# Optimization experiments

Measured on AMD Instinct MI355X. Metric: run time of the kernel, lower is better.

Reference implementation:

```python
import jax, jax.numpy as jnp
import numpy as np

# static multi-scale config (Deformable-DETR encoder, 1024x1024 image, strides 8/16/32/64)
SPATIAL_SHAPES = np.array([[128, 128], [64, 64], [32, 32], [16, 16]])  # (L, 2) = (h, w)
NUM_HEADS, NUM_LEVELS, NUM_POINTS = 8, 4, 4
EMBED, HEAD_DIM = 256, 32
NUM_KEYS = int(SPATIAL_SHAPES.prod(-1).sum())  # 21760


def _grid_sample(img, grid):
    """Bilinear grid_sample, padding_mode='zeros', align_corners=False.
    img: (BH, C, H, W); grid: (BH, Nq, P, 2) in [-1,1] -> (BH, C, Nq, P)."""
    BH, C, H, W = img.shape
    gx = (grid[..., 0] + 1.0) * (W / 2) - 0.5
    gy = (grid[..., 1] + 1.0) * (H / 2) - 0.5
    x0f, y0f = jnp.floor(gx), jnp.floor(gy)
    wx, wy = gx - x0f, gy - y0f
    x0, y0 = x0f.astype(jnp.int32), y0f.astype(jnp.int32)
    flat = img.reshape(BH, C, H * W)

    def gather(xi, yi, w):
        valid = (xi >= 0) & (xi < W) & (yi >= 0) & (yi < H)
        idx = jnp.clip(yi, 0, H - 1) * W + jnp.clip(xi, 0, W - 1)
        g = jnp.take_along_axis(flat, idx.reshape(BH, 1, -1), axis=2)
        g = g.reshape(BH, C, xi.shape[1], xi.shape[2])
        return g * (w * valid)[:, None]

    return (gather(x0, y0, (1 - wx) * (1 - wy)) + gather(x0 + 1, y0, wx * (1 - wy))
            + gather(x0, y0 + 1, (1 - wx) * wy) + gather(x0 + 1, y0 + 1, wx * wy))


def setup_inputs() -> dict:
    key = jax.random.key(0)
    ks = jax.random.split(key, 12)
    bs, nq = 1, NUM_KEYS
    s = 1.0 / np.sqrt(EMBED)
    return {
        "query": jax.random.normal(ks[0], (bs, nq, EMBED), jnp.float32),
        "query_pos": jax.random.normal(ks[1], (bs, nq, EMBED), jnp.float32),
        "value": jax.random.normal(ks[2], (bs, NUM_KEYS, EMBED), jnp.float32),
        "reference_points": jax.random.uniform(ks[3], (bs, nq, NUM_LEVELS, 2), jnp.float32),
        "spatial_shapes": jnp.asarray(SPATIAL_SHAPES, jnp.int32),
        "W_value": jax.random.normal(ks[4], (EMBED, EMBED), jnp.float32) * s,
        "b_value": jnp.zeros((EMBED,), jnp.float32),
        "W_off": jax.random.normal(ks[5], (NUM_HEADS * NUM_LEVELS * NUM_POINTS * 2, EMBED), jnp.float32) * 0.01,
        "b_off": jax.random.normal(ks[6], (NUM_HEADS * NUM_LEVELS * NUM_POINTS * 2,), jnp.float32),
        "W_attn": jax.random.normal(ks[7], (NUM_HEADS * NUM_LEVELS * NUM_POINTS, EMBED), jnp.float32) * s,
        "b_attn": jnp.zeros((NUM_HEADS * NUM_LEVELS * NUM_POINTS,), jnp.float32),
        "W_out": jax.random.normal(ks[8], (EMBED, EMBED), jnp.float32) * s,
        "b_out": jnp.zeros((EMBED,), jnp.float32),
    }


def reference(query, query_pos, value, reference_points, spatial_shapes,
              W_value, b_value, W_off, b_off, W_attn, b_attn, W_out, b_out):
    bs, nq, _ = query.shape
    identity = query
    q = query + query_pos  # pos_add
    v = value @ W_value.T + b_value  # value_proj: (bs, nk, E)
    v = v.reshape(bs, -1, NUM_HEADS, HEAD_DIM)

    offsets = (q @ W_off.T + b_off).reshape(bs, nq, NUM_HEADS, NUM_LEVELS, NUM_POINTS, 2)
    attn = (q @ W_attn.T + b_attn).reshape(bs, nq, NUM_HEADS, NUM_LEVELS * NUM_POINTS)
    attn = jax.nn.softmax(attn, axis=-1).reshape(bs, nq, NUM_HEADS, NUM_LEVELS, NUM_POINTS)

    # offset_normalizer = (w, h) per level; ref points are 2D -> loc = ref + off/norm
    normalizer = jnp.asarray(SPATIAL_SHAPES[:, ::-1].copy(), query.dtype)  # (L, 2)
    loc = reference_points[:, :, None, :, None, :] + offsets / normalizer[None, None, None, :, None, :]
    grids = 2.0 * loc - 1.0  # (bs, nq, H, L, P, 2)

    starts = np.concatenate([[0], np.cumsum(SPATIAL_SHAPES.prod(-1))])
    sampled = []
    for lvl in range(NUM_LEVELS):
        H_, W_ = int(SPATIAL_SHAPES[lvl, 0]), int(SPATIAL_SHAPES[lvl, 1])
        v_l = v[:, int(starts[lvl]):int(starts[lvl + 1])]  # (bs, H*W, heads, Dh)
        v_l = v_l.transpose(0, 2, 3, 1).reshape(bs * NUM_HEADS, HEAD_DIM, H_, W_)
        g_l = grids[:, :, :, lvl].transpose(0, 2, 1, 3, 4).reshape(bs * NUM_HEADS, nq, NUM_POINTS, 2)
        sampled.append(_grid_sample(v_l, g_l))  # (bs*H, Dh, nq, P)
    sampled = jnp.concatenate(sampled, axis=-1)  # (bs*H, Dh, nq, L*P)

    aw = attn.transpose(0, 2, 1, 3, 4).reshape(bs * NUM_HEADS, 1, nq, NUM_LEVELS * NUM_POINTS)
    out = (sampled * aw).sum(-1).reshape(bs, NUM_HEADS * HEAD_DIM, nq).transpose(0, 2, 1)
    out = out @ W_out.T + b_out  # output_proj
    return out + identity  # residual (dropout is identity at eval)
```

## Files before the change

### kernel.cpp

```cpp
#include <hip/hip_runtime.h>
#include <hip/hip_bf16.h>
#include <math.h>
#include <type_traits>

#define K_DIM 256
using bf16 = __hip_bfloat16;

typedef __attribute__((ext_vector_type(8))) short s8v;
typedef __attribute__((ext_vector_type(4))) float f4v;

__device__ __forceinline__ float b2f(unsigned short u) {
    return __uint_as_float(((unsigned)u) << 16);
}
__device__ __forceinline__ unsigned short f2b(float f) {
    unsigned u = __float_as_uint(f);
    unsigned r = 0x7FFFu + ((u >> 16) & 1u);
    return (unsigned short)((u + r) >> 16);
}
__device__ __forceinline__ float  ld1(const float* p) { return *p; }
__device__ __forceinline__ float  ld1(const bf16*  p) { return b2f(*(const unsigned short*)p); }
__device__ __forceinline__ void   st1(float* p, float v) { *p = v; }
__device__ __forceinline__ void   st1(bf16*  p, float v) { *(unsigned short*)p = f2b(v); }
__device__ __forceinline__ float4 ld4(const float* p) { return *(const float4*)p; }
__device__ __forceinline__ float4 ld4(const bf16*  p) {
    ushort4 u = *(const ushort4*)p;
    return make_float4(b2f(u.x), b2f(u.y), b2f(u.z), b2f(u.w));
}
__device__ __forceinline__ s8v ldw8(const bf16* p) { return *(const s8v*)p; }

__device__ __forceinline__ bool detect_bf16(const unsigned* __restrict__ qw) {
    unsigned w = qw[threadIdx.x & 63];
    unsigned t = (w >> 8) & 0x7F;
    bool hit = (t >= 0x3Bu) && (t <= 0x42u);
    unsigned long long m = __ballot(hit);
    return __popcll(m) >= 32;
}

#define P1_TOTAL 164480
__global__ __launch_bounds__(256) void k_prep1(
    const unsigned* __restrict__ qd,
    const void* wv, const void* wo, const void* wa,
    const void* bv, const void* bo, const void* ba, bf16* __restrict__ dst)
{
    const bool isb = detect_bf16(qd);
    const int i4 = (blockIdx.x * 256 + threadIdx.x) * 4;
    if (i4 >= P1_TOTAL) return;
    const void* src; int off;
    if      (i4 < 65536)  { src = wv; off = i4; }
    else if (i4 < 131072) { src = wo; off = i4 - 65536; }
    else if (i4 < 163840) { src = wa; off = i4 - 131072; }
    else if (i4 < 164096) { src = bv; off = i4 - 163840; }
    else if (i4 < 164352) { src = bo; off = i4 - 164096; }
    else                  { src = ba; off = i4 - 164352; }
    if (isb) {
        *(ushort4*)(dst + i4) = *(const ushort4*)((const unsigned short*)src + off);
    } else {
        float4 v = *(const float4*)((const float*)src + off);
        *(ushort4*)(dst + i4) = make_ushort4(f2b(v.x), f2b(v.y), f2b(v.z), f2b(v.w));
    }
}

#define P2_TOTAL 65792
__global__ __launch_bounds__(256) void k_prep2(
    const unsigned* __restrict__ qd,
    const void* wout, const void* bout, bf16* __restrict__ dst)
{
    const bool isb = detect_bf16(qd);
    const int i4 = (blockIdx.x * 256 + threadIdx.x) * 4;
    if (i4 >= P2_TOTAL) return;
    const void* src; int off;
    if (i4 < 65536) { src = wout; off = i4; }
    else            { src = bout; off = i4 - 65536; }
    if (isb) {
        *(ushort4*)(dst + i4) = *(const ushort4*)((const unsigned short*)src + off);
    } else {
        float4 v = *(const float4*)((const float*)src + off);
        *(ushort4*)(dst + i4) = make_ushort4(f2b(v.x), f2b(v.y), f2b(v.z), f2b(v.w));
    }
}

template<typename AT, typename RT, typename CT, int NFRAG, bool ADD_A2, bool SPLIT,
         bool ADD_RES, bool HMAJOR, bool HM2, bool A1HM>
__device__ __forceinline__ void mfma_gemm_body(
    unsigned short* __restrict__ As,
    const AT* __restrict__ A1, const AT* __restrict__ A2,
    const bf16* __restrict__ W1, const bf16* __restrict__ bias1, CT* __restrict__ C1, int N1,
    const bf16* __restrict__ W2, const bf16* __restrict__ bias2, bf16* __restrict__ C2, int N2,
    const RT* __restrict__ Res, int Mtot)
{
    const int tid = threadIdx.x;
    const int bm = blockIdx.x * 32;

    {
        const AT* t1 = A1 + (size_t)bm * K_DIM;
        if constexpr (!ADD_A2 && std::is_same<AT, bf16>::value) {
            #pragma unroll
            for (int j = 0; j < 4; ++j) {
                const int e = j * 2048 + tid * 8;
                const int row = e >> 8, col = e & 255;
                const bf16* src;
                if constexpr (A1HM)
                    src = (const bf16*)A1 +
                          ((size_t)(col >> 5) * (size_t)Mtot + (size_t)(bm + row)) * 32 + (col & 31);
                else
                    src = t1 + e;
                *(s8v*)&As[row * 264 + col] = *(const s8v*)src;
            }
        } else {
            const AT* t2 = ADD_A2 ? (A2 + (size_t)bm * K_DIM) : (const AT*)0;
            #pragma unroll
            for (int j = 0; j < 8; ++j) {
                const int e = j * 1024 + tid * 4;
                float4 v = ld4(t1 + e);
                if (ADD_A2) {
                    float4 w2 = ld4(t2 + e);
                    v.x += w2.x; v.y += w2.y; v.z += w2.z; v.w += w2.w;
                }
                const int row = e >> 8, col = e & 255;
                *(ushort4*)&As[row * 264 + col] =
                    make_ushort4(f2b(v.x), f2b(v.y), f2b(v.z), f2b(v.w));
            }
        }
    }
    __syncthreads();

    const int wv = tid >> 6;
    const int lane = tid & 63;
    const int n15 = lane & 15;
    const int quad = lane >> 4;

    const bf16* Wr[NFRAG];
    int col[NFRAG];
    #pragma unroll
    for (int f = 0; f < NFRAG; ++f) {
        const int c = (wv * NFRAG + f) * 16 + n15;
        col[f] = c;
        if (SPLIT && c >= N1) Wr[f] = W2 + (size_t)(c - N1) * K_DIM;
        else                  Wr[f] = W1 + (size_t)c * K_DIM;
    }

    const f4v zz = {0.f, 0.f, 0.f, 0.f};
    f4v acc[2][NFRAG];
    #pragma unroll
    for (int mi = 0; mi < 2; ++mi)
        #pragma unroll
        for (int f = 0; f < NFRAG; ++f) acc[mi][f] = zz;

    #pragma unroll
    for (int kk = 0; kk < 8; ++kk) {
        const int k0 = kk * 32 + quad * 8;
        s8v b[NFRAG];
        #pragma unroll
        for (int f = 0; f < NFRAG; ++f) b[f] = ldw8(Wr[f] + k0);
        s8v a[2];
        #pragma unroll
        for (int mi = 0; mi < 2; ++mi)
            a[mi] = *(const s8v*)&As[(mi * 16 + n15) * 264 + k0];
        #pragma unroll
        for (int mi = 0; mi < 2; ++mi)
            #pragma unroll
            for (int f = 0; f < NFRAG; ++f)
                acc[mi][f] = __builtin_amdgcn_mfma_f32_16x16x32_bf16(a[mi], b[f], acc[mi][f], 0, 0, 0);
    }

    #pragma unroll
    for (int f = 0; f < NFRAG; ++f) {
        const int c = col[f];
        const bool hi = SPLIT && (c >= N1);
        const int cc = hi ? (c - N1) : c;
        const float bv = hi ? ld1(bias2 + cc) : ld1(bias1 + c);
        size_t hbase = 0;
        if (HMAJOR) hbase = (size_t)(c >> 5) * (size_t)Mtot * 32 + (c & 31);
        size_t hbase2 = 0;
        if (HM2) hbase2 = (size_t)(cc >> 4) * (size_t)Mtot * 16 + (cc & 15);
        #pragma unroll
        for (int mi = 0; mi < 2; ++mi)
            #pragma unroll
            for (int r = 0; r < 4; ++r) {
                const int m = bm + mi * 16 + quad * 4 + r;
                float v = acc[mi][f][r] + bv;
                if (ADD_RES) v += ld1(Res + (size_t)m * N1 + c);
                if (hi) {
                    if (HM2) st1(C2 + hbase2 + (size_t)m * 16, v);
                    else     st1(C2 + (size_t)m * N2 + cc, v);
                }
                else if (HMAJOR) st1(C1 + hbase + (size_t)m * 32, v);
                else             st1(C1 + (size_t)m * N1 + c, v);
            }
    }
}

template<int NFRAG, bool ADD_A2, bool SPLIT, bool HMAJOR, bool HM2>
__global__ __launch_bounds__(256) void k_gemm(
    const unsigned* __restrict__ qd, const void* A1, const void* A2,
    const bf16* W1, const bf16* b1, bf16* C1, int N1,
    const bf16* W2, const bf16* b2, bf16* C2, int N2, int Mtot)
{
    __shared__ unsigned short As[32 * 264];
    if (detect_bf16(qd))
        mfma_gemm_body<bf16, float, bf16, NFRAG, ADD_A2, SPLIT, false, HMAJOR, HM2, false>(As,
            (const bf16*)A1, (const bf16*)A2, W1, b1, C1, N1, W2, b2, C2, N2, nullptr, Mtot);
    else
        mfma_gemm_body<float, float, bf16, NFRAG, ADD_A2, SPLIT, false, HMAJOR, HM2, false>(As,
            (const float*)A1, (const float*)A2, W1, b1, C1, N1, W2, b2, C2, N2, nullptr, Mtot);
}

__global__ __launch_bounds__(256) void k_gemm_final(
    const unsigned* __restrict__ qd, const bf16* A1,
    const bf16* W, const bf16* bias, const void* Res, void* C, int Mtot)
{
    __shared__ unsigned short As[32 * 264];
    if (detect_bf16(qd))
        mfma_gemm_body<bf16, bf16, bf16, 4, false, false, true, false, false, true>(As,
            A1, nullptr, W, bias, (bf16*)C, 256,
            nullptr, nullptr, nullptr, 0, (const bf16*)Res, Mtot);
    else
        mfma_gemm_body<bf16, float, float, 4, false, false, true, false, false, true>(As,
            A1, nullptr, W, bias, (float*)C, 256,
            nullptr, nullptr, nullptr, 0, (const float*)Res, Mtot);
}

struct SampLds {
    float    swgt[16][32][4];
    unsigned sidx[16][32][4];
};

__global__ __launch_bounds__(256) void k_sample(
    const unsigned* __restrict__ qd, const bf16* __restrict__ vproj,
    bf16* __restrict__ osb, const bf16* __restrict__ logits,
    const void* __restrict__ refp, int Mtot)
{
    __shared__ SampLds L;
    const bool isb = detect_bf16(qd);
    const int t  = threadIdx.x;
    const int p  = t >> 3;
    const int dg = t & 7;
    const int head = blockIdx.x & 7;
    const int qc   = blockIdx.x >> 3;
    const int q = qc * 32 + p;
    const size_t hm = (size_t)head * (size_t)Mtot;

    float f0, f1, f2, f3;
    {
        ushort4 u = *(const ushort4*)(osb + (hm + q) * 32 + dg * 4);
        f0 = b2f(u.x); f1 = b2f(u.y); f2 = b2f(u.z); f3 = b2f(u.w);
    }

    float p0, p1;
    {
        ushort2 lu = *(const ushort2*)(logits + (hm + q) * 16 + dg * 2);
        float l0 = b2f(lu.x), l1 = b2f(lu.y);
        float mx = fmaxf(l0, l1);
        mx = fmaxf(mx, __shfl_xor(mx, 1));
        mx = fmaxf(mx, __shfl_xor(mx, 2));
        mx = fmaxf(mx, __shfl_xor(mx, 4));
        float e0 = __expf(l0 - mx), e1 = __expf(l1 - mx);
        float s = e0 + e1;
        s += __shfl_xor(s, 1);
        s += __shfl_xor(s, 2);
        s += __shfl_xor(s, 4);
        const float inv = 1.f / s;
        p0 = e0 * inv; p1 = e1 * inv;
    }

    const int lv = dg >> 1;
    float rx, ry;
    if (isb) {
        rx = ld1((const bf16*)refp + (size_t)q * 8 + 2 * lv);
        ry = ld1((const bf16*)refp + (size_t)q * 8 + 2 * lv + 1);
    } else {
        rx = ld1((const float*)refp + (size_t)q * 8 + 2 * lv);
        ry = ld1((const float*)refp + (size_t)q * 8 + 2 * lv + 1);
    }

    #pragma unroll
    for (int tt = 0; tt < 2; ++tt) {
        const int i = dg * 2 + tt;
        const int l = i >> 2;
        const int WW = 128 >> l;
        const int st = (l == 0) ? 0 : (l == 1) ? 16384 : (l == 2) ? 20480 : 21504;
        const float ox = tt ? f2 : f0;
        const float oy = tt ? f3 : f1;
        const float aw = tt ? p1 : p0;
        const float gx = rx * (float)WW + ox - 0.5f;
        const float gy = ry * (float)WW + oy - 0.5f;
        const float x0f = floorf(gx);
        const float y0f = floorf(gy);
        const float wx = gx - x0f;
        const float wy = gy - y0f;
        const int x0 = (int)x0f;
        const int y0 = (int)y0f;
        const float vx0 = (x0 >= 0 && x0 < WW) ? 1.f : 0.f;
        const float vx1 = (x0 + 1 >= 0 && x0 + 1 < WW) ? 1.f : 0.f;
        const float vy0 = (y0 >= 0 && y0 < WW) ? 1.f : 0.f;
        const float vy1 = (y0 + 1 >= 0 && y0 + 1 < WW) ? 1.f : 0.f;
        const int xc0 = min(max(x0, 0), WW - 1);
        const int xc1 = min(max(x0 + 1, 0), WW - 1);
        const int yc0 = min(max(y0, 0), WW - 1);
        const int yc1 = min(max(y0 + 1, 0), WW - 1);
        *(float4*)L.swgt[i][p] = make_float4(
            (1.f - wx) * (1.f - wy) * aw * vx0 * vy0,
            wx * (1.f - wy) * aw * vx1 * vy0,
            (1.f - wx) * wy * aw * vx0 * vy1,
            wx * wy * aw * vx1 * vy1);
        *(uint4*)L.sidx[i][p] = make_uint4(
            (unsigned)(st + yc0 * WW + xc0) * 64u,
            (unsigned)(st + yc0 * WW + xc1) * 64u,
            (unsigned)(st + yc1 * WW + xc0) * 64u,
            (unsigned)(st + yc1 * WW + xc1) * 64u);
    }
    __syncthreads();

    const unsigned hb = (unsigned)(hm * 64) + (unsigned)dg * 8u;
    const char* vb = (const char*)vproj;
    float a0 = 0.f, a1 = 0.f, a2 = 0.f, a3 = 0.f;
    #pragma unroll
    for (int i = 0; i < 16; ++i) {
        const uint4  iv = *(const uint4*)L.sidx[i][p];
        const float4 wv = *(const float4*)L.swgt[i][p];
        {
            ushort4 pv = *(const ushort4*)(vb + (size_t)(iv.x + hb));
            a0 = fmaf(wv.x, b2f(pv.x), a0); a1 = fmaf(wv.x, b2f(pv.y), a1);
            a2 = fmaf(wv.x, b2f(pv.z), a2); a3 = fmaf(wv.x, b2f(pv.w), a3);
        }
        {
            ushort4 pv = *(const ushort4*)(vb + (size_t)(iv.y + hb));
            a0 = fmaf(wv.y, b2f(pv.x), a0); a1 = fmaf(wv.y, b2f(pv.y), a1);
            a2 = fmaf(wv.y, b2f(pv.z), a2); a3 = fmaf(wv.y, b2f(pv.w), a3);
        }
        {
            ushort4 pv = *(const ushort4*)(vb + (size_t)(iv.z + hb));
            a0 = fmaf(wv.z, b2f(pv.x), a0); a1 = fmaf(wv.z, b2f(pv.y), a1);
            a2 = fmaf(wv.z, b2f(pv.z), a2); a3 = fmaf(wv.z, b2f(pv.w), a3);
        }
        {
            ushort4 pv = *(const ushort4*)(vb + (size_t)(iv.w + hb));
            a0 = fmaf(wv.w, b2f(pv.x), a0); a1 = fmaf(wv.w, b2f(pv.y), a1);
            a2 = fmaf(wv.w, b2f(pv.z), a2); a3 = fmaf(wv.w, b2f(pv.w), a3);
        }
    }
    *(ushort4*)(osb + (hm + q) * 32 + dg * 4) =
        make_ushort4(f2b(a0), f2b(a1), f2b(a2), f2b(a3));
}

extern "C" void kernel_launch(void* const* d_in, const int* in_sizes, int n_in,
                              void* d_out, int out_size, void* d_ws, size_t ws_size,
                              hipStream_t stream) {
    const void* query     = d_in[0];
    const void* query_pos = d_in[1];
    const void* value     = d_in[2];
    const void* refp      = d_in[3];
    const void* W_value = d_in[5];
    const void* b_value = d_in[6];
    const void* W_off   = d_in[7];
    const void* b_off   = d_in[8];
    const void* W_attn  = d_in[9];
    const void* b_attn  = d_in[10];
    const void* W_out   = d_in[11];
    const void* b_out   = d_in[12];
    const unsigned* qd = (const unsigned*)d_in[0];

    const int M = in_sizes[0] / 256;
    char* wsb = (char*)d_ws;

    bf16* vproj = (bf16*)wsb;
    bf16* osb   = (bf16*)(wsb + (size_t)M * 512);
    bf16* logit = (bf16*)d_out;
    bf16* wc1   = (bf16*)((char*)d_out + (8u << 20));
    const bf16* c_wv = wc1;
    const bf16* c_wo = wc1 + 65536;
    const bf16* c_wa = wc1 + 131072;
    const bf16* c_bv = wc1 + 163840;
    const bf16* c_bo = wc1 + 164096;
    const bf16* c_ba = wc1 + 164352;
    bf16* wc2 = vproj;

    dim3 blk(256, 1, 1);
    dim3 g32((unsigned)(M / 32), 1, 1);
    dim3 gs((unsigned)(M / 4), 1, 1);

    k_prep1<<<dim3((P1_TOTAL / 4 + 255) / 256), blk, 0, stream>>>(qd,
        W_value, W_off, W_attn, b_value, b_off, b_attn, wc1);
    k_gemm<4, false, false, true, false><<<g32, blk, 0, stream>>>(qd, value, nullptr,
        c_wv, c_bv, vproj, 256, nullptr, nullptr, nullptr, 0, M);
    k_gemm<6, true, true, true, true><<<g32, blk, 0, stream>>>(qd, query, query_pos,
        c_wo, c_bo, osb, 256, c_wa, c_ba, logit, 128, M);
    k_sample<<<gs, blk, 0, stream>>>(qd, vproj, osb, logit, refp, M);
    k_prep2<<<dim3((P2_TOTAL / 4 + 255) / 256), blk, 0, stream>>>(qd, W_out, b_out, wc2);
    k_gemm_final<<<g32, blk, 0, stream>>>(qd, osb, wc2, wc2 + 65536, query, d_out, M);
}
```

Before: 223.6 us.

## Gather horizontal bilinear neighbours with one wide load split across lanes

The bilinear sampler relies on the x0 and x0+1 pixels being contiguous in the value projection. Lanes 0-3 of each 8-lane group now load 16 bytes (8 channels) from the left pixel, and lanes 4-7 load from the right pixel. Each thread issues two gathers per sample instead of four, and the LDS index table shrinks to two entries. All 32 loads are issued before any FMA to raise memory-level parallelism. A cross-lane shuffle adds the two column halves. The cost is more registers, plus a possible read one pixel past the end of the buffer when x0 is clamped at the last column, since that read gets zero weight but still touches memory.

```diff
diff --git a/kernel.cpp b/kernel.cpp
--- a/kernel.cpp
+++ b/kernel.cpp
@@ -222,7 +222,7 @@
 
 struct SampLds {
     float    swgt[16][32][4];
-    unsigned sidx[16][32][4];
+    unsigned sidx[16][32][2];
 };
 
 __global__ __launch_bounds__(256) void k_sample(
@@ -290,57 +290,62 @@
         const float wy = gy - y0f;
         const int x0 = (int)x0f;
         const int y0 = (int)y0f;
-        const float vx0 = (x0 >= 0 && x0 < WW) ? 1.f : 0.f;
-        const float vx1 = (x0 + 1 >= 0 && x0 + 1 < WW) ? 1.f : 0.f;
+        const float ux0 = (x0 >= 0 && x0 < WW) ? (1.f - wx) : 0.f;
+        const float ux1 = (x0 + 1 >= 0 && x0 + 1 < WW) ? wx : 0.f;
+        const float uA = (x0 >= 0) ? ux0 : ux1;
+        const float uB = (x0 >= 0) ? ux1 : 0.f;
+        const int bx = min(max(x0, 0), WW - 1);
         const float vy0 = (y0 >= 0 && y0 < WW) ? 1.f : 0.f;
         const float vy1 = (y0 + 1 >= 0 && y0 + 1 < WW) ? 1.f : 0.f;
-        const int xc0 = min(max(x0, 0), WW - 1);
-        const int xc1 = min(max(x0 + 1, 0), WW - 1);
         const int yc0 = min(max(y0, 0), WW - 1);
         const int yc1 = min(max(y0 + 1, 0), WW - 1);
-        *(float4*)L.swgt[i][p] = make_float4(
-            (1.f - wx) * (1.f - wy) * aw * vx0 * vy0,
-            wx * (1.f - wy) * aw * vx1 * vy0,
-            (1.f - wx) * wy * aw * vx0 * vy1,
-            wx * wy * aw * vx1 * vy1);
-        *(uint4*)L.sidx[i][p] = make_uint4(
-            (unsigned)(st + yc0 * WW + xc0) * 64u,
-            (unsigned)(st + yc0 * WW + xc1) * 64u,
-            (unsigned)(st + yc1 * WW + xc0) * 64u,
-            (unsigned)(st + yc1 * WW + xc1) * 64u);
+        const float cy0 = (1.f - wy) * vy0 * aw;
+        const float cy1 = wy * vy1 * aw;
+        *(float4*)L.swgt[i][p] = make_float4(uA * cy0, uB * cy0, uA * cy1, uB * cy1);
+        *(uint2*)L.sidx[i][p] = make_uint2(
+            (unsigned)(st + yc0 * WW + bx) * 64u,
+            (unsigned)(st + yc1 * WW + bx) * 64u);
     }
     __syncthreads();
 
-    const unsigned hb = (unsigned)(hm * 64) + (unsigned)dg * 8u;
+    const unsigned hb = (unsigned)(hm * 64) + (unsigned)dg * 16u;
     const char* vb = (const char*)vproj;
-    float a0 = 0.f, a1 = 0.f, a2 = 0.f, a3 = 0.f;
+
+    uint2 iv[16];
+    #pragma unroll
+    for (int i = 0; i < 16; ++i) iv[i] = *(const uint2*)L.sidx[i][p];
+
+    s8v r0[16], r1[16];
     #pragma unroll
     for (int i = 0; i < 16; ++i) {
-        const uint4  iv = *(const uint4*)L.sidx[i][p];
-        const float4 wv = *(const float4*)L.swgt[i][p];
-        {
-            ushort4 pv = *(const ushort4*)(vb + (size_t)(iv.x + hb));
-            a0 = fmaf(wv.x, b2f(pv.x), a0); a1 = fmaf(wv.x, b2f(pv.y), a1);
-            a2 = fmaf(wv.x, b2f(pv.z), a2); a3 = fmaf(wv.x, b2f(pv.w), a3);
-        }
-        {
-            ushort4 pv = *(const ushort4*)(vb + (size_t)(iv.y + hb));
-            a0 = fmaf(wv.y, b2f(pv.x), a0); a1 = fmaf(wv.y, b2f(pv.y), a1);
-            a2 = fmaf(wv.y, b2f(pv.z), a2); a3 = fmaf(wv.y, b2f(pv.w), a3);
-        }
-        {
-            ushort4 pv = *(const ushort4*)(vb + (size_t)(iv.z + hb));
-            a0 = fmaf(wv.z, b2f(pv.x), a0); a1 = fmaf(wv.z, b2f(pv.y), a1);
-            a2 = fmaf(wv.z, b2f(pv.z), a2); a3 = fmaf(wv.z, b2f(pv.w), a3);
-        }
-        {
-            ushort4 pv = *(const ushort4*)(vb + (size_t)(iv.w + hb));
-            a0 = fmaf(wv.w, b2f(pv.x), a0); a1 = fmaf(wv.w, b2f(pv.y), a1);
-            a2 = fmaf(wv.w, b2f(pv.z), a2); a3 = fmaf(wv.w, b2f(pv.w), a3);
-        }
-    }
-    *(ushort4*)(osb + (hm + q) * 32 + dg * 4) =
-        make_ushort4(f2b(a0), f2b(a1), f2b(a2), f2b(a3));
+        r0[i] = *(const s8v*)(vb + (size_t)(iv[i].x + hb));
+        r1[i] = *(const s8v*)(vb + (size_t)(iv[i].y + hb));
+    }
+
+    const bool lo = (dg < 4);
+    float acc[8] = {0.f, 0.f, 0.f, 0.f, 0.f, 0.f, 0.f, 0.f};
+    #pragma unroll
+    for (int i = 0; i < 16; ++i) {
+        const float4 w = *(const float4*)L.swgt[i][p];
+        const float w0 = lo ? w.x : w.y;
+        const float w1 = lo ? w.z : w.w;
+        #pragma unroll
+        for (int k = 0; k < 8; ++k)
+            acc[k] = fmaf(w0, b2f((unsigned short)r0[i][k]), acc[k]);
+        #pragma unroll
+        for (int k = 0; k < 8; ++k)
+            acc[k] = fmaf(w1, b2f((unsigned short)r1[i][k]), acc[k]);
+    }
+
+    #pragma unroll
+    for (int k = 0; k < 8; ++k) acc[k] += __shfl_xor(acc[k], 4);
+
+    if (dg < 4) {
+        s8v o;
+        #pragma unroll
+        for (int k = 0; k < 8; ++k) o[k] = (short)f2b(acc[k]);
+        *(s8v*)(osb + (hm + q) * 32 + dg * 8) = o;
+    }
 }
 
 extern "C" void kernel_launch(void* const* d_in, const int* in_sizes, int n_in,
```

Result: faster. 206.0 us (-7.9%).
